# Kernel optimization log

Hardware: AMD Instinct MI355X
Metric: run time of the kernel (lower is better)

## Reference

```python
import jax, jax.numpy as jnp
import numpy as np

N = 100000
E = 1250000
IN_C = 64
HID = 128
OUT_C = 64
K = 10
ALPHA = 0.1


def setup_inputs() -> dict:
    key = jax.random.key(0)
    ks = jax.random.split(key, 10)
    s = 1.0 / np.sqrt(IN_C)
    sh = 1.0 / np.sqrt(HID)
    return {
        "x": jax.random.normal(ks[0], (N, IN_C), jnp.float32),
        "edge_attr": jax.random.normal(ks[1], (E, IN_C), jnp.float32),
        "W_node": jax.random.uniform(ks[2], (IN_C, HID), jnp.float32, -s, s),
        "b_node": jnp.zeros((HID,), jnp.float32),
        "W_edge": jax.random.uniform(ks[3], (IN_C, HID), jnp.float32, -s, s),
        "b_edge": jnp.zeros((HID,), jnp.float32),
        "W1": jax.random.uniform(ks[4], (HID, HID), jnp.float32, -sh, sh),
        "b1": jnp.zeros((HID,), jnp.float32),
        "W2": jax.random.uniform(ks[5], (HID, OUT_C), jnp.float32, -sh, sh),
        "b2": jnp.zeros((OUT_C,), jnp.float32),
        "edge_index": jax.random.randint(ks[6], (2, E), 0, N, jnp.int32),
    }


def _appnp(h0, edge_index):
    # PyG APPNP with gcn_norm (adds self-loops, symmetric normalization).
    src = jnp.concatenate([edge_index[0], jnp.arange(N, dtype=edge_index.dtype)])
    dst = jnp.concatenate([edge_index[1], jnp.arange(N, dtype=edge_index.dtype)])
    ew = jnp.ones(src.shape, h0.dtype)
    deg = jax.ops.segment_sum(ew, dst, num_segments=N)
    dinv = jnp.where(deg > 0, jax.lax.rsqrt(jnp.maximum(deg, 1e-12)), 0.0)
    norm = (dinv[src] * dinv[dst])[:, None]  # [(E+N),1]

    def step(h, _):
        agg = jax.ops.segment_sum(norm * h[src], dst, num_segments=N)
        return (1.0 - ALPHA) * agg + ALPHA * h0, None

    h, _ = jax.lax.scan(step, h0, None, length=K)
    return h


def reference(x, edge_attr, W_node, b_node, W_edge, b_edge, W1, b1, W2, b2, edge_index):
    x_node = x @ W_node + b_node            # [N, HID]
    e_emb = edge_attr @ W_edge + b_edge     # [E, HID]
    # add self loops with zero edge embeddings
    ar = jnp.arange(N, dtype=edge_index.dtype)
    row = jnp.concatenate([edge_index[0], ar])
    col = jnp.concatenate([edge_index[1], ar])
    e_emb_loop = jnp.concatenate([e_emb, jnp.zeros((N, HID), e_emb.dtype)], axis=0)
    msg = x_node[col] + e_emb_loop           # [(E+N), HID]
    ssum = jax.ops.segment_sum(msg, row, num_segments=N)
    cnt = jax.ops.segment_sum(jnp.ones(row.shape, x.dtype), row, num_segments=N)
    x_enh = ssum / jnp.maximum(cnt, 1.0)[:, None]  # scatter mean (cnt>=1 via loops)
    x_enh = jax.nn.relu(x_enh)               # dropout = identity in eval
    h = jax.nn.relu(x_enh @ W1 + b1)
    h0 = h @ W2 + b2                         # [N, OUT_C]
    return _appnp(h0, edge_index)
```

## Files before the change

### kernel.cpp

```cpp
#include <hip/hip_runtime.h>
#include <hip/hip_bf16.h>

#define N_NODES 100000
#define E_EDGES 1250000
#define INC 64
#define HIDC 128
#define OUTC 64
#define K_ITERS 10
#define ALPHA 0.1f

__global__ __launch_bounds__(256) void hist2(const int* __restrict__ ei,
                                             int* __restrict__ degRow,
                                             int* __restrict__ degDst) {
    int e = blockIdx.x * 256 + threadIdx.x;
    if (e >= E_EDGES) return;
    atomicAdd(&degRow[ei[e]], 1);
    atomicAdd(&degDst[ei[E_EDGES + e]], 1);
}

__global__ __launch_bounds__(256) void dinv_kernel(const int* __restrict__ degDst,
                                                   float* __restrict__ dinv) {
    int i = blockIdx.x * 256 + threadIdx.x;
    if (i >= N_NODES) return;
    dinv[i] = rsqrtf((float)(degDst[i] + 1));
}

__global__ __launch_bounds__(256) void scan_block_sums2(const int* __restrict__ degRow,
                                                        const int* __restrict__ degDst,
                                                        int* __restrict__ blockSums) {
    const int* deg = blockIdx.y ? degDst : degRow;
    __shared__ int sh[256];
    int t = threadIdx.x;
    int i = blockIdx.x * 256 + t;
    sh[t] = (i < N_NODES) ? deg[i] : 0;
    __syncthreads();
    for (int off = 128; off > 0; off >>= 1) {
        if (t < off) sh[t] += sh[t + off];
        __syncthreads();
    }
    if (t == 0) blockSums[blockIdx.y * 512 + blockIdx.x] = sh[0];
}

__global__ __launch_bounds__(512) void scan_top2(const int* __restrict__ blockSums,
                                                 int* __restrict__ blockScan, int nb) {
    const int* bs = blockSums + blockIdx.x * 512;
    int* bo = blockScan + blockIdx.x * 512;
    __shared__ int sh[512];
    int t = threadIdx.x;
    int v = (t < nb) ? bs[t] : 0;
    sh[t] = v;
    __syncthreads();
    for (int off = 1; off < 512; off <<= 1) {
        int xv = (t >= off) ? sh[t - off] : 0;
        __syncthreads();
        sh[t] += xv;
        __syncthreads();
    }
    if (t < nb) bo[t] = sh[t] - v;
}

__global__ __launch_bounds__(256) void scan_write_rp2(const int* __restrict__ degRow,
                                                      const int* __restrict__ degDst,
                                                      const int* __restrict__ blockScan,
                                                      int* __restrict__ rpRow,
                                                      int* __restrict__ rpDst) {
    const int* deg = blockIdx.y ? degDst : degRow;
    int* rp = blockIdx.y ? rpDst : rpRow;
    __shared__ int sh[256];
    int t = threadIdx.x;
    int i = blockIdx.x * 256 + t;
    int v = (i < N_NODES) ? deg[i] : 0;
    sh[t] = v;
    __syncthreads();
    for (int off = 1; off < 256; off <<= 1) {
        int xv = (t >= off) ? sh[t - off] : 0;
        __syncthreads();
        sh[t] += xv;
        __syncthreads();
    }
    if (i < N_NODES) rp[i] = blockScan[blockIdx.y * 512 + blockIdx.x] + (sh[t] - v);
    if (i == 0) rp[N_NODES] = E_EDGES;
}

__global__ __launch_bounds__(256) void scatter_both(const int* __restrict__ ei,
                                                    const float* __restrict__ dinv,
                                                    const int* __restrict__ rpRow,
                                                    const int* __restrict__ rpDst,
                                                    int* __restrict__ curRow,
                                                    int* __restrict__ curDst,
                                                    int2* __restrict__ ce,
                                                    int2* __restrict__ ew) {
    int e = blockIdx.x * 256 + threadIdx.x;
    if (e >= E_EDGES) return;
    int r0 = ei[e];
    int r1 = ei[E_EDGES + e];
    int pr = rpRow[r0] + atomicAdd(&curRow[r0], 1);
    ce[pr] = make_int2(r1, e);
    int pd = rpDst[r1] + atomicAdd(&curDst[r1], 1);
    float w = (1.0f - ALPHA) * dinv[r0] * dinv[r1];
    ew[pd] = make_int2(r0, __float_as_int(w));
}

__global__ __launch_bounds__(256) void aggregate(const float* __restrict__ x,
                                                 const float* __restrict__ ea,
                                                 const int* __restrict__ rpRow,
                                                 const int2* __restrict__ ce,
                                                 float* __restrict__ S,
                                                 float* __restrict__ cntRow) {
    int wid = (blockIdx.x * 256 + threadIdx.x) >> 6;
    int lane = threadIdx.x & 63;
    if (wid >= N_NODES) return;
    int jb = rpRow[wid], je = rpRow[wid + 1];
    float ax0 = x[(size_t)wid * 64 + lane], ax1 = 0.f, ax2 = 0.f, ax3 = 0.f;
    float ae0 = 0.f, ae1 = 0.f, ae2 = 0.f, ae3 = 0.f;
    int j = jb;
    for (; j + 3 < je; j += 4) {
        int2 c0 = ce[j], c1 = ce[j + 1], c2 = ce[j + 2], c3 = ce[j + 3];
        ax0 += x[(size_t)c0.x * 64 + lane];
        ax1 += x[(size_t)c1.x * 64 + lane];
        ax2 += x[(size_t)c2.x * 64 + lane];
        ax3 += x[(size_t)c3.x * 64 + lane];
        ae0 += ea[(size_t)c0.y * 64 + lane];
        ae1 += ea[(size_t)c1.y * 64 + lane];
        ae2 += ea[(size_t)c2.y * 64 + lane];
        ae3 += ea[(size_t)c3.y * 64 + lane];
    }
    for (; j < je; ++j) {
        int2 c = ce[j];
        ax0 += x[(size_t)c.x * 64 + lane];
        ae0 += ea[(size_t)c.y * 64 + lane];
    }
    S[(size_t)wid * 128 + lane] = (ax0 + ax1) + (ax2 + ax3);
    S[(size_t)wid * 128 + 64 + lane] = (ae0 + ae1) + (ae2 + ae3);
    if (lane == 0) cntRow[wid] = (float)(je - jb + 1);
}

template <int NC, int MODE>
__global__ __launch_bounds__(256) void gemm_k(const float* __restrict__ A,
                                              const float* __restrict__ Wa,
                                              const float* __restrict__ Wb,
                                              const float* __restrict__ ba,
                                              const float* __restrict__ bb,
                                              const float* __restrict__ cnt,
                                              float* __restrict__ out) {
    constexpr int CPT = NC / 16;
    __shared__ float Al[64][132];
    __shared__ float Wl[64][NC];
    const int tid = threadIdx.x;
    const int rb = blockIdx.x * 64;

    for (int idx = tid; idx < 64 * 32; idx += 256) {
        int r = idx >> 5, c4 = idx & 31;
        int gr = rb + r;
        float4 v = make_float4(0.f, 0.f, 0.f, 0.f);
        if (gr < N_NODES) v = *reinterpret_cast<const float4*>(A + (size_t)gr * 128 + c4 * 4);
        *reinterpret_cast<float4*>(&Al[r][c4 * 4]) = v;
    }

    const int trow = tid >> 4, tcol = tid & 15;
    float acc[4][CPT];
#pragma unroll
    for (int q = 0; q < 4; q++)
#pragma unroll
        for (int j = 0; j < CPT; j++) acc[q][j] = 0.f;

    for (int half = 0; half < 2; ++half) {
        __syncthreads();
        for (int idx = tid; idx < 64 * (NC / 4); idx += 256) {
            int k = idx / (NC / 4), c4 = idx % (NC / 4);
            int gk = half * 64 + k;
            const float* src;
            if constexpr (MODE == 0) {
                src = (gk < 64) ? (Wa + (size_t)gk * NC + c4 * 4)
                                : (Wb + (size_t)(gk - 64) * NC + c4 * 4);
            } else {
                src = Wa + (size_t)gk * NC + c4 * 4;
            }
            *reinterpret_cast<float4*>(&Wl[k][c4 * 4]) = *reinterpret_cast<const float4*>(src);
        }
        __syncthreads();
#pragma unroll 4
        for (int k = 0; k < 64; k++) {
            float a0 = Al[trow][half * 64 + k];
            float a1 = Al[trow + 16][half * 64 + k];
            float a2 = Al[trow + 32][half * 64 + k];
            float a3 = Al[trow + 48][half * 64 + k];
#pragma unroll
            for (int j = 0; j < CPT; j++) {
                float w = Wl[k][j * 16 + tcol];
                acc[0][j] += a0 * w;
                acc[1][j] += a1 * w;
                acc[2][j] += a2 * w;
                acc[3][j] += a3 * w;
            }
        }
    }

#pragma unroll
    for (int q = 0; q < 4; q++) {
        int gr = rb + trow + 16 * q;
        if (gr >= N_NODES) continue;
        float inv = 0.f;
        if constexpr (MODE == 0) inv = 1.0f / cnt[gr];
#pragma unroll
        for (int j = 0; j < CPT; j++) {
            int c = j * 16 + tcol;
            float v = acc[q][j];
            if constexpr (MODE == 0) {
                v = v * inv + ba[c] + (1.0f - inv) * bb[c];
                v = fmaxf(v, 0.f);
            } else if constexpr (MODE == 1) {
                v = fmaxf(v + ba[c], 0.f);
            } else {
                v = v + ba[c];
            }
            out[(size_t)gr * NC + c] = v;
        }
    }
}

__global__ __launch_bounds__(256) void appnp_step(const float* __restrict__ h,
                                                  const float* __restrict__ h0,
                                                  float* __restrict__ out,
                                                  const int* __restrict__ rp,
                                                  const int2* __restrict__ ew,
                                                  const float* __restrict__ dinv) {
    int wid = (blockIdx.x * 256 + threadIdx.x) >> 6;
    int lane = threadIdx.x & 63;
    if (wid >= N_NODES) return;
    float di = dinv[wid];
    float acc0 = (1.0f - ALPHA) * di * di * h[(size_t)wid * 64 + lane];
    float acc1 = 0.f, acc2 = 0.f, acc3 = 0.f;
    int e = rp[wid], eend = rp[wid + 1];
    for (; e + 3 < eend; e += 4) {
        int2 w0 = ew[e], w1 = ew[e + 1], w2 = ew[e + 2], w3 = ew[e + 3];
        acc0 += __int_as_float(w0.y) * h[(size_t)w0.x * 64 + lane];
        acc1 += __int_as_float(w1.y) * h[(size_t)w1.x * 64 + lane];
        acc2 += __int_as_float(w2.y) * h[(size_t)w2.x * 64 + lane];
        acc3 += __int_as_float(w3.y) * h[(size_t)w3.x * 64 + lane];
    }
    for (; e < eend; ++e) {
        int2 w = ew[e];
        acc0 += __int_as_float(w.y) * h[(size_t)w.x * 64 + lane];
    }
    out[(size_t)wid * 64 + lane] =
        ((acc0 + acc1) + (acc2 + acc3)) + ALPHA * h0[(size_t)wid * 64 + lane];
}

extern "C" void kernel_launch(void* const* d_in, const int* in_sizes, int n_in,
                              void* d_out, int out_size, void* d_ws, size_t ws_size,
                              hipStream_t stream) {
    const float* x      = (const float*)d_in[0];
    const float* eattr  = (const float*)d_in[1];
    const float* W_node = (const float*)d_in[2];
    const float* b_node = (const float*)d_in[3];
    const float* W_edge = (const float*)d_in[4];
    const float* b_edge = (const float*)d_in[5];
    const float* W1     = (const float*)d_in[6];
    const float* b1     = (const float*)d_in[7];
    const float* W2     = (const float*)d_in[8];
    const float* b2     = (const float*)d_in[9];
    const int*   ei     = (const int*)d_in[10];
    float* out = (float*)d_out;

    char* ws = (char*)d_ws;
    size_t off = 0;
    auto alloc = [&](size_t bytes) -> void* {
        void* p = ws + off;
        off += (bytes + 511) & ~(size_t)511;
        return p;
    };
    float* buf0   = (float*)alloc((size_t)N_NODES * 128 * 4);
    float* h0     = (float*)alloc((size_t)N_NODES * 64 * 4);
    int2*  ew     = (int2*)alloc((size_t)E_EDGES * 8);
    float* cntRow = (float*)alloc((size_t)N_NODES * 4);
    int*   zeros4 = (int*)alloc((size_t)4 * N_NODES * 4);
    float* dinv   = (float*)alloc((size_t)N_NODES * 4);
    int*   rpRow  = (int*)alloc((size_t)(N_NODES + 1) * 4);
    int*   rpDst  = (int*)alloc((size_t)(N_NODES + 1) * 4);
    int*   blockSums = (int*)alloc(1024 * 4);
    int*   blockScan = (int*)alloc(1024 * 4);

    int* degRow = zeros4;
    int* degDst = zeros4 + N_NODES;
    int* curRow = zeros4 + 2 * N_NODES;
    int* curDst = zeros4 + 3 * N_NODES;

    int2* ce = (int2*)h0;

    constexpr int NB = (N_NODES + 255) / 256;

    hipMemsetAsync(zeros4, 0, (size_t)4 * N_NODES * 4, stream);

    hist2<<<(E_EDGES + 255) / 256, 256, 0, stream>>>(ei, degRow, degDst);
    dinv_kernel<<<(N_NODES + 255) / 256, 256, 0, stream>>>(degDst, dinv);

    scan_block_sums2<<<dim3(NB, 2), 256, 0, stream>>>(degRow, degDst, blockSums);
    scan_top2<<<2, 512, 0, stream>>>(blockSums, blockScan, NB);
    scan_write_rp2<<<dim3(NB, 2), 256, 0, stream>>>(degRow, degDst, blockScan, rpRow, rpDst);

    scatter_both<<<(E_EDGES + 255) / 256, 256, 0, stream>>>(ei, dinv, rpRow, rpDst,
                                                            curRow, curDst, ce, ew);

    aggregate<<<(N_NODES + 3) / 4, 256, 0, stream>>>(x, eattr, rpRow, ce, buf0, cntRow);

    gemm_k<128, 0><<<(N_NODES + 63) / 64, 256, 0, stream>>>(buf0, W_node, W_edge, b_node, b_edge, cntRow, buf0);
    gemm_k<128, 1><<<(N_NODES + 63) / 64, 256, 0, stream>>>(buf0, W1, nullptr, b1, nullptr, nullptr, buf0);
    gemm_k<64, 2><<<(N_NODES + 63) / 64, 256, 0, stream>>>(buf0, W2, nullptr, b2, nullptr, nullptr, h0);

    float* hA = buf0;
    float* hB = buf0 + (size_t)N_NODES * 64;
    const float* hcur = h0;
    for (int k = 0; k < K_ITERS; k++) {
        float* dst = (k == K_ITERS - 1) ? out : ((k & 1) ? hB : hA);
        appnp_step<<<(N_NODES * 64 + 255) / 256, 256, 0, stream>>>(hcur, h0, dst, rpDst, ew, dinv);
        hcur = dst;
    }
}
```

Baseline: 1.194 ms.

## Balance edge work across a fixed number of waves and transpose GEMM weight tiles

Adds a partition kernel that binary-searches the CSR row pointers so each of 16384 waves handles a contiguous range of nodes with roughly equal edge counts. The aggregate and APPNP step kernels now loop over those node ranges instead of assigning one wave per node. This aims to cut per-wave launch and tail overhead and even out the load. Separately, the GEMM kernel now stages A in 64-column halves and stores W transposed in shared memory so the inner loop can use float4 LDS reads. The transposed weight staging uses strided scalar global loads, and each wave now walks its nodes serially, so per-wave latency hiding may be reduced.

```diff
diff --git a/kernel.cpp b/kernel.cpp
--- a/kernel.cpp
+++ b/kernel.cpp
@@ -8,6 +8,7 @@
 #define OUTC 64
 #define K_ITERS 10
 #define ALPHA 0.1f
+#define NWAVES 16384
 
 __global__ __launch_bounds__(256) void hist2(const int* __restrict__ ei,
                                              int* __restrict__ degRow,
@@ -80,6 +81,24 @@
     }
     if (i < N_NODES) rp[i] = blockScan[blockIdx.y * 512 + blockIdx.x] + (sh[t] - v);
     if (i == 0) rp[N_NODES] = E_EDGES;
+}
+
+__global__ __launch_bounds__(256) void partition_waves(const int* __restrict__ rpRow,
+                                                       const int* __restrict__ rpDst,
+                                                       int* __restrict__ nsRow,
+                                                       int* __restrict__ nsDst) {
+    int w = blockIdx.x * 256 + threadIdx.x;
+    if (w > NWAVES) return;
+    const int* rp = blockIdx.y ? rpDst : rpRow;
+    int* ns = blockIdx.y ? nsDst : nsRow;
+    if (w == NWAVES) { ns[w] = N_NODES; return; }
+    long long target = (long long)w * E_EDGES / NWAVES;
+    int lo = 0, hi = N_NODES;
+    while (lo < hi) {
+        int mid = (lo + hi) >> 1;
+        if ((long long)rp[mid] >= target) hi = mid; else lo = mid + 1;
+    }
+    ns[w] = lo;
 }
 
 __global__ __launch_bounds__(256) void scatter_both(const int* __restrict__ ei,
@@ -105,34 +124,39 @@
                                                  const float* __restrict__ ea,
                                                  const int* __restrict__ rpRow,
                                                  const int2* __restrict__ ce,
+                                                 const int* __restrict__ nsRow,
                                                  float* __restrict__ S,
                                                  float* __restrict__ cntRow) {
-    int wid = (blockIdx.x * 256 + threadIdx.x) >> 6;
+    int w = (blockIdx.x * 256 + threadIdx.x) >> 6;
     int lane = threadIdx.x & 63;
-    if (wid >= N_NODES) return;
-    int jb = rpRow[wid], je = rpRow[wid + 1];
-    float ax0 = x[(size_t)wid * 64 + lane], ax1 = 0.f, ax2 = 0.f, ax3 = 0.f;
-    float ae0 = 0.f, ae1 = 0.f, ae2 = 0.f, ae3 = 0.f;
-    int j = jb;
-    for (; j + 3 < je; j += 4) {
-        int2 c0 = ce[j], c1 = ce[j + 1], c2 = ce[j + 2], c3 = ce[j + 3];
-        ax0 += x[(size_t)c0.x * 64 + lane];
-        ax1 += x[(size_t)c1.x * 64 + lane];
-        ax2 += x[(size_t)c2.x * 64 + lane];
-        ax3 += x[(size_t)c3.x * 64 + lane];
-        ae0 += ea[(size_t)c0.y * 64 + lane];
-        ae1 += ea[(size_t)c1.y * 64 + lane];
-        ae2 += ea[(size_t)c2.y * 64 + lane];
-        ae3 += ea[(size_t)c3.y * 64 + lane];
-    }
-    for (; j < je; ++j) {
-        int2 c = ce[j];
-        ax0 += x[(size_t)c.x * 64 + lane];
-        ae0 += ea[(size_t)c.y * 64 + lane];
-    }
-    S[(size_t)wid * 128 + lane] = (ax0 + ax1) + (ax2 + ax3);
-    S[(size_t)wid * 128 + 64 + lane] = (ae0 + ae1) + (ae2 + ae3);
-    if (lane == 0) cntRow[wid] = (float)(je - jb + 1);
+    int n0 = nsRow[w], n1 = nsRow[w + 1];
+    if (n0 >= n1) return;
+    int j = rpRow[n0];
+    for (int n = n0; n < n1; ++n) {
+        int je = rpRow[n + 1];
+        int deg = je - j;
+        float ax0 = x[(size_t)n * 64 + lane], ax1 = 0.f, ax2 = 0.f, ax3 = 0.f;
+        float ae0 = 0.f, ae1 = 0.f, ae2 = 0.f, ae3 = 0.f;
+        for (; j + 3 < je; j += 4) {
+            int2 c0 = ce[j], c1 = ce[j + 1], c2 = ce[j + 2], c3 = ce[j + 3];
+            ax0 += x[(size_t)c0.x * 64 + lane];
+            ax1 += x[(size_t)c1.x * 64 + lane];
+            ax2 += x[(size_t)c2.x * 64 + lane];
+            ax3 += x[(size_t)c3.x * 64 + lane];
+            ae0 += ea[(size_t)c0.y * 64 + lane];
+            ae1 += ea[(size_t)c1.y * 64 + lane];
+            ae2 += ea[(size_t)c2.y * 64 + lane];
+            ae3 += ea[(size_t)c3.y * 64 + lane];
+        }
+        for (; j < je; ++j) {
+            int2 c = ce[j];
+            ax0 += x[(size_t)c.x * 64 + lane];
+            ae0 += ea[(size_t)c.y * 64 + lane];
+        }
+        S[(size_t)n * 128 + lane] = (ax0 + ax1) + (ax2 + ax3);
+        S[(size_t)n * 128 + 64 + lane] = (ae0 + ae1) + (ae2 + ae3);
+        if (lane == 0) cntRow[n] = (float)(deg + 1);
+    }
 }
 
 template <int NC, int MODE>
@@ -144,20 +168,12 @@
                                               const float* __restrict__ cnt,
                                               float* __restrict__ out) {
     constexpr int CPT = NC / 16;
-    __shared__ float Al[64][132];
-    __shared__ float Wl[64][NC];
+    __shared__ float Al[64][68];
+    __shared__ float Wt[NC][68];
     const int tid = threadIdx.x;
     const int rb = blockIdx.x * 64;
-
-    for (int idx = tid; idx < 64 * 32; idx += 256) {
-        int r = idx >> 5, c4 = idx & 31;
-        int gr = rb + r;
-        float4 v = make_float4(0.f, 0.f, 0.f, 0.f);
-        if (gr < N_NODES) v = *reinterpret_cast<const float4*>(A + (size_t)gr * 128 + c4 * 4);
-        *reinterpret_cast<float4*>(&Al[r][c4 * 4]) = v;
-    }
-
     const int trow = tid >> 4, tcol = tid & 15;
+
     float acc[4][CPT];
 #pragma unroll
     for (int q = 0; q < 4; q++)
@@ -166,32 +182,41 @@
 
     for (int half = 0; half < 2; ++half) {
         __syncthreads();
-        for (int idx = tid; idx < 64 * (NC / 4); idx += 256) {
-            int k = idx / (NC / 4), c4 = idx % (NC / 4);
-            int gk = half * 64 + k;
-            const float* src;
-            if constexpr (MODE == 0) {
-                src = (gk < 64) ? (Wa + (size_t)gk * NC + c4 * 4)
-                                : (Wb + (size_t)(gk - 64) * NC + c4 * 4);
-            } else {
-                src = Wa + (size_t)gk * NC + c4 * 4;
-            }
-            *reinterpret_cast<float4*>(&Wl[k][c4 * 4]) = *reinterpret_cast<const float4*>(src);
-        }
-        __syncthreads();
-#pragma unroll 4
-        for (int k = 0; k < 64; k++) {
-            float a0 = Al[trow][half * 64 + k];
-            float a1 = Al[trow + 16][half * 64 + k];
-            float a2 = Al[trow + 32][half * 64 + k];
-            float a3 = Al[trow + 48][half * 64 + k];
+        for (int idx = tid; idx < 64 * 16; idx += 256) {
+            int r = idx >> 4, c4 = idx & 15;
+            int gr = rb + r;
+            float4 v = make_float4(0.f, 0.f, 0.f, 0.f);
+            if (gr < N_NODES)
+                v = *reinterpret_cast<const float4*>(A + (size_t)gr * 128 + half * 64 + c4 * 4);
+            *reinterpret_cast<float4*>(&Al[r][c4 * 4]) = v;
+        }
+        const float* Wbase;
+        if constexpr (MODE == 0) Wbase = half ? Wb : Wa;
+        else Wbase = Wa + (size_t)half * 64 * NC;
+        for (int idx = tid; idx < NC * 16; idx += 256) {
+            int c = idx % NC;
+            int k4 = idx / NC;
+            float4 wv;
+            wv.x = Wbase[(size_t)(k4 * 4 + 0) * NC + c];
+            wv.y = Wbase[(size_t)(k4 * 4 + 1) * NC + c];
+            wv.z = Wbase[(size_t)(k4 * 4 + 2) * NC + c];
+            wv.w = Wbase[(size_t)(k4 * 4 + 3) * NC + c];
+            *reinterpret_cast<float4*>(&Wt[c][k4 * 4]) = wv;
+        }
+        __syncthreads();
+#pragma unroll
+        for (int k4 = 0; k4 < 16; ++k4) {
+            float4 a0 = *reinterpret_cast<const float4*>(&Al[trow][k4 * 4]);
+            float4 a1 = *reinterpret_cast<const float4*>(&Al[trow + 16][k4 * 4]);
+            float4 a2 = *reinterpret_cast<const float4*>(&Al[trow + 32][k4 * 4]);
+            float4 a3 = *reinterpret_cast<const float4*>(&Al[trow + 48][k4 * 4]);
 #pragma unroll
             for (int j = 0; j < CPT; j++) {
-                float w = Wl[k][j * 16 + tcol];
-                acc[0][j] += a0 * w;
-                acc[1][j] += a1 * w;
-                acc[2][j] += a2 * w;
-                acc[3][j] += a3 * w;
+                float4 wv = *reinterpret_cast<const float4*>(&Wt[j * 16 + tcol][k4 * 4]);
+                acc[0][j] += a0.x * wv.x + a0.y * wv.y + a0.z * wv.z + a0.w * wv.w;
+                acc[1][j] += a1.x * wv.x + a1.y * wv.y + a1.z * wv.z + a1.w * wv.w;
+                acc[2][j] += a2.x * wv.x + a2.y * wv.y + a2.z * wv.z + a2.w * wv.w;
+                acc[3][j] += a3.x * wv.x + a3.y * wv.y + a3.z * wv.z + a3.w * wv.w;
             }
         }
     }
@@ -224,27 +249,32 @@
                                                   float* __restrict__ out,
                                                   const int* __restrict__ rp,
                                                   const int2* __restrict__ ew,
-                                                  const float* __restrict__ dinv) {
-    int wid = (blockIdx.x * 256 + threadIdx.x) >> 6;
+                                                  const float* __restrict__ dinv,
+                                                  const int* __restrict__ ns) {
+    int w = (blockIdx.x * 256 + threadIdx.x) >> 6;
     int lane = threadIdx.x & 63;
-    if (wid >= N_NODES) return;
-    float di = dinv[wid];
-    float acc0 = (1.0f - ALPHA) * di * di * h[(size_t)wid * 64 + lane];
-    float acc1 = 0.f, acc2 = 0.f, acc3 = 0.f;
-    int e = rp[wid], eend = rp[wid + 1];
-    for (; e + 3 < eend; e += 4) {
-        int2 w0 = ew[e], w1 = ew[e + 1], w2 = ew[e + 2], w3 = ew[e + 3];
-        acc0 += __int_as_float(w0.y) * h[(size_t)w0.x * 64 + lane];
-        acc1 += __int_as_float(w1.y) * h[(size_t)w1.x * 64 + lane];
-        acc2 += __int_as_float(w2.y) * h[(size_t)w2.x * 64 + lane];
-        acc3 += __int_as_float(w3.y) * h[(size_t)w3.x * 64 + lane];
-    }
-    for (; e < eend; ++e) {
-        int2 w = ew[e];
-        acc0 += __int_as_float(w.y) * h[(size_t)w.x * 64 + lane];
-    }
-    out[(size_t)wid * 64 + lane] =
-        ((acc0 + acc1) + (acc2 + acc3)) + ALPHA * h0[(size_t)wid * 64 + lane];
+    int n0 = ns[w], n1 = ns[w + 1];
+    if (n0 >= n1) return;
+    int e = rp[n0];
+    for (int n = n0; n < n1; ++n) {
+        int eend = rp[n + 1];
+        float di = dinv[n];
+        float acc0 = (1.0f - ALPHA) * di * di * h[(size_t)n * 64 + lane];
+        float acc1 = 0.f, acc2 = 0.f, acc3 = 0.f;
+        for (; e + 3 < eend; e += 4) {
+            int2 w0 = ew[e], w1 = ew[e + 1], w2 = ew[e + 2], w3 = ew[e + 3];
+            acc0 += __int_as_float(w0.y) * h[(size_t)w0.x * 64 + lane];
+            acc1 += __int_as_float(w1.y) * h[(size_t)w1.x * 64 + lane];
+            acc2 += __int_as_float(w2.y) * h[(size_t)w2.x * 64 + lane];
+            acc3 += __int_as_float(w3.y) * h[(size_t)w3.x * 64 + lane];
+        }
+        for (; e < eend; ++e) {
+            int2 wv = ew[e];
+            acc0 += __int_as_float(wv.y) * h[(size_t)wv.x * 64 + lane];
+        }
+        out[(size_t)n * 64 + lane] =
+            ((acc0 + acc1) + (acc2 + acc3)) + ALPHA * h0[(size_t)n * 64 + lane];
+    }
 }
 
 extern "C" void kernel_launch(void* const* d_in, const int* in_sizes, int n_in,
@@ -278,6 +308,8 @@
     float* dinv   = (float*)alloc((size_t)N_NODES * 4);
     int*   rpRow  = (int*)alloc((size_t)(N_NODES + 1) * 4);
     int*   rpDst  = (int*)alloc((size_t)(N_NODES + 1) * 4);
+    int*   nsRow  = (int*)alloc((size_t)(NWAVES + 1) * 4);
+    int*   nsDst  = (int*)alloc((size_t)(NWAVES + 1) * 4);
     int*   blockSums = (int*)alloc(1024 * 4);
     int*   blockScan = (int*)alloc(1024 * 4);
 
@@ -299,10 +331,12 @@
     scan_top2<<<2, 512, 0, stream>>>(blockSums, blockScan, NB);
     scan_write_rp2<<<dim3(NB, 2), 256, 0, stream>>>(degRow, degDst, blockScan, rpRow, rpDst);
 
+    partition_waves<<<dim3((NWAVES + 256) / 256, 2), 256, 0, stream>>>(rpRow, rpDst, nsRow, nsDst);
+
     scatter_both<<<(E_EDGES + 255) / 256, 256, 0, stream>>>(ei, dinv, rpRow, rpDst,
                                                             curRow, curDst, ce, ew);
 
-    aggregate<<<(N_NODES + 3) / 4, 256, 0, stream>>>(x, eattr, rpRow, ce, buf0, cntRow);
+    aggregate<<<NWAVES / 4, 256, 0, stream>>>(x, eattr, rpRow, ce, nsRow, buf0, cntRow);
 
     gemm_k<128, 0><<<(N_NODES + 63) / 64, 256, 0, stream>>>(buf0, W_node, W_edge, b_node, b_edge, cntRow, buf0);
     gemm_k<128, 1><<<(N_NODES + 63) / 64, 256, 0, stream>>>(buf0, W1, nullptr, b1, nullptr, nullptr, buf0);
@@ -313,7 +347,7 @@
     const float* hcur = h0;
     for (int k = 0; k < K_ITERS; k++) {
         float* dst = (k == K_ITERS - 1) ? out : ((k & 1) ? hB : hA);
-        appnp_step<<<(N_NODES * 64 + 255) / 256, 256, 0, stream>>>(hcur, h0, dst, rpDst, ew, dinv);
+        appnp_step<<<NWAVES / 4, 256, 0, stream>>>(hcur, h0, dst, rpDst, ew, dinv, nsDst);
         hcur = dst;
     }
 }
```

After: 1.387 ms. 16.2% more time.
